# Performance work log

Measured on AMD Instinct MI355X. Metric: run time of the kernel, lower is better.

Reference implementation:

```python
import jax, jax.numpy as jnp
import numpy as np

B, L, C, OUT = 8, 256, 512, 512


def setup_inputs() -> dict:
    key = jax.random.key(0)
    ks = jax.random.split(key, 8)
    xd = jax.random.normal(ks[0], (B, L, C), jnp.float32)
    xt = jax.random.normal(ks[1], (B, L, C), jnp.float32)
    # Linear weights stored (in, out): y = x @ W + b (equiv. to torch x @ W^T)
    Wc = jax.random.normal(ks[2], (C, C), jnp.float32) * 0.02
    bc = jnp.zeros((C,), jnp.float32)
    Wp = jax.random.normal(ks[3], (C, C), jnp.float32) * 0.02
    bp = jnp.zeros((C,), jnp.float32)
    Wf = jax.random.normal(ks[4], (C, OUT), jnp.float32) * 0.02
    bf = jnp.zeros((OUT,), jnp.float32)
    return {"xd": xd, "xt": xt, "Wc": Wc, "bc": bc, "Wp": Wp, "bp": bp, "Wf": Wf, "bf": bf}


def reference(xd, xt, Wc, bc, Wp, bp, Wf, bf):
    # projected features
    pt = jax.nn.relu(xt) @ Wp + bp              # (b, Lt, C)
    pc = jax.nn.relu(xd) @ Wc + bc              # (b, Ld, C)
    # sigmoid bilinear scores: (b, Lt, Ld) == (b, Ld, Lt) since Lt == Ld structurally
    scores = jax.nn.sigmoid(jnp.einsum('bic,bkc->bik', pt, pc))
    # normalize by total per-batch sum
    w = scores / jnp.sum(scores, axis=(1, 2), keepdims=True)
    # tanh of elementwise outer product, reduced with attention weights
    # cp[b,c] = sum_{i,j} tanh(xd[b,i,c] * xt[b,j,c]) * w[b,i,j]
    cp = jnp.einsum('bijc,bij->bc', jnp.tanh(xd[:, :, None, :] * xt[:, None, :, :]), w)
    return cp @ Wf + bf
```

## Files before the change

kernel.cpp:

```cpp
#include <hip/hip_runtime.h>
#include <math.h>

#define B_   8
#define L_   256
#define C_   512
#define OUT_ 512

typedef _Float16 half8 __attribute__((ext_vector_type(8)));
typedef float    f32x4 __attribute__((ext_vector_type(4)));

__global__ __launch_bounds__(256)
void wconv_kernel(const float* __restrict__ Wp, const float* __restrict__ Wc,
                  _Float16* __restrict__ hWp, _Float16* __restrict__ hWc)
{
    const int which = blockIdx.z;
    const float* __restrict__ W = which ? Wc : Wp;
    _Float16* __restrict__ H    = which ? hWc : hWp;
    __shared__ float tl[32][33];
    const int k0 = blockIdx.y << 5, n0 = blockIdx.x << 5;
    const int tr = threadIdx.x >> 5, tc = threadIdx.x & 31;
    #pragma unroll
    for (int i = 0; i < 32; i += 8)
        tl[tr + i][tc] = W[(size_t)(k0 + tr + i) * C_ + n0 + tc];
    __syncthreads();
    #pragma unroll
    for (int i = 0; i < 32; i += 8)
        H[(size_t)(n0 + tr + i) * C_ + k0 + tc] = (_Float16)tl[tc][tr + i];
}

__global__ __launch_bounds__(256)
void proj_mfma_kernel(const float* __restrict__ xt, const _Float16* __restrict__ hWp,
                      const float* __restrict__ bp,
                      const float* __restrict__ xd, const _Float16* __restrict__ hWc,
                      const float* __restrict__ bc,
                      _Float16* __restrict__ pt, _Float16* __restrict__ pc)
{
    const int which = blockIdx.z;
    const float*    __restrict__ X    = which ? xd : xt;
    const _Float16* __restrict__ W    = which ? hWc : hWp;
    const float*    __restrict__ bias = which ? bc : bp;
    _Float16*       __restrict__ Y    = which ? pc : pt;

    __shared__ _Float16 Ah[2][64][40];
    __shared__ _Float16 Bh[2][64][40];
    __shared__ _Float16 Ot[64][72];

    const int tid = threadIdx.x;
    const int m0 = blockIdx.y << 6, n0 = blockIdx.x << 6;
    const int srow = tid >> 2, sch = (tid & 3) << 3;
    const int lane = tid & 63, wv = tid >> 6;
    const int l15 = lane & 15, quad = lane >> 4;

    const float*    Ag = X + (size_t)(m0 + srow) * C_ + sch;
    const _Float16* Bg = W + (size_t)(n0 + srow) * C_ + sch;

    float4 a0 = *(const float4*)(Ag);
    float4 a1 = *(const float4*)(Ag + 4);
    half8  bv = *(const half8*)(Bg);

    {
        half8 av;
        av[0] = (_Float16)fmaxf(a0.x, 0.f); av[1] = (_Float16)fmaxf(a0.y, 0.f);
        av[2] = (_Float16)fmaxf(a0.z, 0.f); av[3] = (_Float16)fmaxf(a0.w, 0.f);
        av[4] = (_Float16)fmaxf(a1.x, 0.f); av[5] = (_Float16)fmaxf(a1.y, 0.f);
        av[6] = (_Float16)fmaxf(a1.z, 0.f); av[7] = (_Float16)fmaxf(a1.w, 0.f);
        *(half8*)&Ah[0][srow][sch] = av;
        *(half8*)&Bh[0][srow][sch] = bv;
    }

    f32x4 acc[4] = {};
    for (int ks = 0; ks < 16; ++ks) {
        const int cur = ks & 1;
        if (ks < 15) {
            Ag += 32; Bg += 32;
            a0 = *(const float4*)(Ag);
            a1 = *(const float4*)(Ag + 4);
            bv = *(const half8*)(Bg);
        }
        __syncthreads();
        half8 af = *(const half8*)&Ah[cur][(wv << 4) + l15][quad << 3];
        #pragma unroll
        for (int nb = 0; nb < 4; ++nb) {
            half8 bf = *(const half8*)&Bh[cur][(nb << 4) + l15][quad << 3];
            acc[nb] = __builtin_amdgcn_mfma_f32_16x16x32_f16(af, bf, acc[nb], 0, 0, 0);
        }
        if (ks < 15) {
            half8 av;
            av[0] = (_Float16)fmaxf(a0.x, 0.f); av[1] = (_Float16)fmaxf(a0.y, 0.f);
            av[2] = (_Float16)fmaxf(a0.z, 0.f); av[3] = (_Float16)fmaxf(a0.w, 0.f);
            av[4] = (_Float16)fmaxf(a1.x, 0.f); av[5] = (_Float16)fmaxf(a1.y, 0.f);
            av[6] = (_Float16)fmaxf(a1.z, 0.f); av[7] = (_Float16)fmaxf(a1.w, 0.f);
            *(half8*)&Ah[cur ^ 1][srow][sch] = av;
            *(half8*)&Bh[cur ^ 1][srow][sch] = bv;
        }
    }

    __syncthreads();
    #pragma unroll
    for (int nb = 0; nb < 4; ++nb) {
        const float bz = bias[n0 + (nb << 4) + l15];
        #pragma unroll
        for (int r = 0; r < 4; ++r)
            Ot[(wv << 4) + (quad << 2) + r][(nb << 4) + l15] = (_Float16)(acc[nb][r] + bz);
    }
    __syncthreads();
    const int erow = tid >> 3, ech = (tid & 7) << 3;
    #pragma unroll
    for (int h = 0; h < 64; h += 32)
        *(half8*)&Y[(size_t)(m0 + erow + h) * C_ + n0 + ech] = *(const half8*)&Ot[erow + h][ech];
}

__global__ __launch_bounds__(256)
void sc_gemm_mfma_kernel(const _Float16* __restrict__ pt, const _Float16* __restrict__ pc,
                         float* __restrict__ dotb)
{
    const int b = blockIdx.z >> 2, ks4 = blockIdx.z & 3;
    const _Float16* __restrict__ A  = pt + (size_t)b * L_ * C_ + (ks4 << 7);
    const _Float16* __restrict__ Bm = pc + (size_t)b * L_ * C_ + (ks4 << 7);
    float* __restrict__ D = dotb + (size_t)ks4 * (B_ * L_ * L_) + (size_t)b * (L_ * L_);

    __shared__ _Float16 Ah[2][64][40];
    __shared__ _Float16 Bh[2][64][40];

    const int tid = threadIdx.x;
    const int m0 = blockIdx.y << 6, n0 = blockIdx.x << 6;
    const int srow = tid >> 2, sch = (tid & 3) << 3;
    const int lane = tid & 63, wv = tid >> 6;
    const int l15 = lane & 15, quad = lane >> 4;

    const _Float16* Ag = A  + (size_t)(m0 + srow) * C_ + sch;
    const _Float16* Bg = Bm + (size_t)(n0 + srow) * C_ + sch;

    half8 av = *(const half8*)Ag;
    half8 bv = *(const half8*)Bg;
    *(half8*)&Ah[0][srow][sch] = av;
    *(half8*)&Bh[0][srow][sch] = bv;

    f32x4 acc[4] = {};
    for (int t = 0; t < 4; ++t) {
        const int cur = t & 1;
        if (t < 3) {
            Ag += 32; Bg += 32;
            av = *(const half8*)Ag;
            bv = *(const half8*)Bg;
        }
        __syncthreads();
        half8 af = *(const half8*)&Ah[cur][(wv << 4) + l15][quad << 3];
        #pragma unroll
        for (int nb = 0; nb < 4; ++nb) {
            half8 bf = *(const half8*)&Bh[cur][(nb << 4) + l15][quad << 3];
            acc[nb] = __builtin_amdgcn_mfma_f32_16x16x32_f16(af, bf, acc[nb], 0, 0, 0);
        }
        if (t < 3) {
            *(half8*)&Ah[cur ^ 1][srow][sch] = av;
            *(half8*)&Bh[cur ^ 1][srow][sch] = bv;
        }
    }
    #pragma unroll
    for (int nb = 0; nb < 4; ++nb)
        #pragma unroll
        for (int r = 0; r < 4; ++r)
            D[(size_t)(m0 + (wv << 4) + (quad << 2) + r) * L_ + n0 + (nb << 4) + l15] = acc[nb][r];
}

__global__ __launch_bounds__(256)
void sc_finish_kernel(float* __restrict__ dotb, float* __restrict__ sums_part)
{
    __shared__ float red[256];
    const int bl = blockIdx.x;
    const int b  = bl >> 6;
    const size_t off = (size_t)b * (L_ * L_) + (size_t)((bl & 63) << 10) + ((size_t)threadIdx.x << 2);
    float4 d = *(const float4*)&dotb[off];
    #pragma unroll
    for (int k = 1; k < 4; ++k) {
        float4 e = *(const float4*)&dotb[(size_t)k * (B_ * L_ * L_) + off];
        d.x += e.x; d.y += e.y; d.z += e.z; d.w += e.w;
    }
    float4 s;
    s.x = 1.0f / (1.0f + expf(-d.x));
    s.y = 1.0f / (1.0f + expf(-d.y));
    s.z = 1.0f / (1.0f + expf(-d.z));
    s.w = 1.0f / (1.0f + expf(-d.w));
    *(float4*)&dotb[off] = s;
    red[threadIdx.x] = (s.x + s.y) + (s.z + s.w);
    __syncthreads();
    for (int st = 128; st > 0; st >>= 1) {
        if (threadIdx.x < st) red[threadIdx.x] += red[threadIdx.x + st];
        __syncthreads();
    }
    if (threadIdx.x == 0) sums_part[bl] = red[0];
}

__device__ __forceinline__ float sig2r(float a) {
    float e = __builtin_amdgcn_exp2f(a);
    return __builtin_amdgcn_rcpf(e + 1.0f);
}

__global__ __launch_bounds__(256, 4)
void cp_partial_kernel(const float* __restrict__ xd, const float* __restrict__ xt,
                       const float* __restrict__ scores, float* __restrict__ partials)
{
    const int i0  = blockIdx.x << 5;
    const int j0  = blockIdx.y << 4;
    const int b   = blockIdx.z >> 1;
    const int tid = threadIdx.x;
    const int c   = ((blockIdx.z & 1) << 8) | tid;

    __shared__ float ws_[16][36];

    const float* __restrict__ sb = scores + (size_t)b * L_ * L_;
    {
        const int jj = tid & 15;
        const int ib = (tid >> 4) << 1;
        #pragma unroll
        for (int r = 0; r < 2; ++r)
            ws_[jj][ib + r] = sb[(size_t)(i0 + ib + r) * L_ + j0 + jj];
    }

    float xds[32], xtv[16];
    const float* __restrict__ xdb = xd + ((size_t)(b * L_ + i0)) * C_ + c;
    const float* __restrict__ xtb = xt + ((size_t)(b * L_ + j0)) * C_ + c;
    #pragma unroll
    for (int i = 0; i < 32; ++i)
        xds[i] = xdb[(size_t)i * C_] * 2.8853900817779268f;
    #pragma unroll
    for (int j = 0; j < 16; ++j)
        xtv[j] = xtb[(size_t)j * C_];
    __syncthreads();

    float a0 = 0.f, a1 = 0.f, a2 = 0.f, a3 = 0.f;
    #pragma unroll 2
    for (int jj = 0; jj < 16; ++jj) {
        const float xv = xtv[jj];
        #pragma unroll
        for (int i = 0; i < 32; i += 4) {
            const float4 w4 = *(const float4*)&ws_[jj][i];
            a0 = fmaf(w4.x, sig2r(xds[i + 0] * xv), a0);
            a1 = fmaf(w4.y, sig2r(xds[i + 1] * xv), a1);
            a2 = fmaf(w4.z, sig2r(xds[i + 2] * xv), a2);
            a3 = fmaf(w4.w, sig2r(xds[i + 3] * xv), a3);
        }
    }
    const int p = ((int)blockIdx.x << 4) | (int)blockIdx.y;
    partials[(size_t)((b << 7) | p) * C_ + c] = (a0 + a1) + (a2 + a3);
}

__global__ __launch_bounds__(512)
void finalize_kernel(const float* __restrict__ partials, const float* __restrict__ sums_part,
                     const float* __restrict__ Wf, const float* __restrict__ bfv,
                     float* __restrict__ out)
{
    const int b = blockIdx.y;
    const int t = threadIdx.x;
    __shared__ float cp[C_];
    __shared__ float red[512];
    __shared__ float sumsh;

    red[t] = (t < 64) ? sums_part[(b << 6) | t] : 0.f;

    float s = 0.f;
    #pragma unroll
    for (int p = 0; p < 128; ++p)
        s += partials[(size_t)((b << 7) | p) * C_ + t];

    __syncthreads();
    for (int st = 256; st > 0; st >>= 1) {
        if (t < st) red[t] += red[t + st];
        __syncthreads();
    }
    if (t == 0) sumsh = red[0];
    __syncthreads();

    cp[t] = 1.0f - 2.0f * s / sumsh;
    __syncthreads();

    const int o  = ((int)blockIdx.x << 6) | (t & 63);
    const int c0 = (t >> 6) << 6;
    float acc = 0.f;
    #pragma unroll 8
    for (int i = 0; i < 64; ++i) {
        const int cc = c0 + i;
        acc = fmaf(cp[cc], Wf[(size_t)cc * OUT_ + o], acc);
    }
    red[t] = acc;
    __syncthreads();
    if (t < 64) {
        float a = 0.f;
        #pragma unroll
        for (int g = 0; g < 8; ++g) a += red[(g << 6) | t];
        out[(size_t)b * OUT_ + o] = a + bfv[o];
    }
}

extern "C" void kernel_launch(void* const* d_in, const int* in_sizes, int n_in,
                              void* d_out, int out_size, void* d_ws, size_t ws_size,
                              hipStream_t stream)
{
    const float* xd = (const float*)d_in[0];
    const float* xt = (const float*)d_in[1];
    const float* Wc = (const float*)d_in[2];
    const float* bc = (const float*)d_in[3];
    const float* Wp = (const float*)d_in[4];
    const float* bp = (const float*)d_in[5];
    const float* Wf = (const float*)d_in[6];
    const float* bf = (const float*)d_in[7];
    float* out = (float*)d_out;

    _Float16* hWp = (_Float16*)d_ws;
    _Float16* hWc = hWp + 262144;
    _Float16* pt  = hWc + 262144;
    _Float16* pc  = pt + 1048576;
    float* dotb      = (float*)(pc + 1048576);
    float* sums_part = dotb + 4 * (B_ * L_ * L_);
    float* partials  = (float*)pt;

    wconv_kernel<<<dim3(16, 16, 2), 256, 0, stream>>>(Wp, Wc, hWp, hWc);
    proj_mfma_kernel<<<dim3(8, 32, 2), 256, 0, stream>>>(xt, hWp, bp, xd, hWc, bc, pt, pc);
    sc_gemm_mfma_kernel<<<dim3(4, 4, 32), 256, 0, stream>>>(pt, pc, dotb);
    sc_finish_kernel<<<512, 256, 0, stream>>>(dotb, sums_part);
    cp_partial_kernel<<<dim3(8, 16, 16), 256, 0, stream>>>(xd, xt, dotb, partials);
    finalize_kernel<<<dim3(8, 8), 512, 0, stream>>>(partials, sums_part, Wf, bf, out);
}
```

Baseline: 153.9 us.

## Fuse score GEMM, sigmoid, sum and cp partial reduction into one kernel

Replaces the split-K score GEMM, the sigmoid/sum finish kernel and the cp partial kernel with a single kernel. Each block computes its 32x32 score tile with MFMA, applies the sigmoid, writes per-block sums, then runs the tanh-weighted reduction over all 512 channels. The tile becomes 32x32 in place of 32x16, which halves the number of partials. It also shares one reciprocal between two sigmoid evaluations. This removes the round trip of the 4-way split-K dot buffer through global memory and two launches, but only 4 of the 8 waves do MFMA work and the GEMM is serialized over 16 K-steps.

```diff
diff --git a/kernel.cpp b/kernel.cpp
--- a/kernel.cpp
+++ b/kernel.cpp
@@ -7,6 +7,7 @@
 #define OUT_ 512
 
 typedef _Float16 half8 __attribute__((ext_vector_type(8)));
+typedef _Float16 half4 __attribute__((ext_vector_type(4)));
 typedef float    f32x4 __attribute__((ext_vector_type(4)));
 
 __global__ __launch_bounds__(256)
@@ -110,139 +111,104 @@
         *(half8*)&Y[(size_t)(m0 + erow + h) * C_ + n0 + ech] = *(const half8*)&Ot[erow + h][ech];
 }
 
-__global__ __launch_bounds__(256)
-void sc_gemm_mfma_kernel(const _Float16* __restrict__ pt, const _Float16* __restrict__ pc,
-                         float* __restrict__ dotb)
-{
-    const int b = blockIdx.z >> 2, ks4 = blockIdx.z & 3;
-    const _Float16* __restrict__ A  = pt + (size_t)b * L_ * C_ + (ks4 << 7);
-    const _Float16* __restrict__ Bm = pc + (size_t)b * L_ * C_ + (ks4 << 7);
-    float* __restrict__ D = dotb + (size_t)ks4 * (B_ * L_ * L_) + (size_t)b * (L_ * L_);
-
-    __shared__ _Float16 Ah[2][64][40];
-    __shared__ _Float16 Bh[2][64][40];
-
+__device__ __forceinline__ float sigmoid_fast(float z) {
+    float e = __builtin_amdgcn_exp2f(-1.4426950408889634f * z);
+    return __builtin_amdgcn_rcpf(e + 1.0f);
+}
+
+__global__ __launch_bounds__(512, 4)
+void cp_scores_kernel(const _Float16* __restrict__ pt, const _Float16* __restrict__ pc,
+                      const float* __restrict__ xd, const float* __restrict__ xt,
+                      float* __restrict__ partials, float* __restrict__ sums_part)
+{
+    const int bx = blockIdx.x, by = blockIdx.y, b = blockIdx.z;
+    const int i0 = bx << 5, j0 = by << 5;
     const int tid = threadIdx.x;
-    const int m0 = blockIdx.y << 6, n0 = blockIdx.x << 6;
-    const int srow = tid >> 2, sch = (tid & 3) << 3;
     const int lane = tid & 63, wv = tid >> 6;
     const int l15 = lane & 15, quad = lane >> 4;
 
-    const _Float16* Ag = A  + (size_t)(m0 + srow) * C_ + sch;
-    const _Float16* Bg = Bm + (size_t)(n0 + srow) * C_ + sch;
-
-    half8 av = *(const half8*)Ag;
-    half8 bv = *(const half8*)Bg;
-    *(half8*)&Ah[0][srow][sch] = av;
-    *(half8*)&Bh[0][srow][sch] = bv;
-
-    f32x4 acc[4] = {};
-    for (int t = 0; t < 4; ++t) {
-        const int cur = t & 1;
-        if (t < 3) {
-            Ag += 32; Bg += 32;
-            av = *(const half8*)Ag;
-            bv = *(const half8*)Bg;
-        }
+    __shared__ _Float16 Ah[2][32][40];
+    __shared__ _Float16 Bh[2][32][40];
+    __shared__ float ws_[32][36];
+    __shared__ float wred[4];
+
+    const int sHalf = tid >> 8;
+    const int srow  = (tid & 255) >> 3;
+    const int sch   = (tid & 7) << 2;
+    const _Float16* Sg = (sHalf ? pc + (size_t)(b * L_ + j0 + srow) * C_
+                                : pt + (size_t)(b * L_ + i0 + srow) * C_) + sch;
+
+    half4 v = *(const half4*)Sg;
+    if (sHalf) *(half4*)&Bh[0][srow][sch] = v; else *(half4*)&Ah[0][srow][sch] = v;
+
+    f32x4 acc = {};
+    for (int ks = 0; ks < 16; ++ks) {
+        const int cur = ks & 1;
+        if (ks < 15) { Sg += 32; v = *(const half4*)Sg; }
         __syncthreads();
-        half8 af = *(const half8*)&Ah[cur][(wv << 4) + l15][quad << 3];
-        #pragma unroll
-        for (int nb = 0; nb < 4; ++nb) {
-            half8 bf = *(const half8*)&Bh[cur][(nb << 4) + l15][quad << 3];
-            acc[nb] = __builtin_amdgcn_mfma_f32_16x16x32_f16(af, bf, acc[nb], 0, 0, 0);
-        }
-        if (t < 3) {
-            *(half8*)&Ah[cur ^ 1][srow][sch] = av;
-            *(half8*)&Bh[cur ^ 1][srow][sch] = bv;
-        }
-    }
-    #pragma unroll
-    for (int nb = 0; nb < 4; ++nb)
-        #pragma unroll
-        for (int r = 0; r < 4; ++r)
-            D[(size_t)(m0 + (wv << 4) + (quad << 2) + r) * L_ + n0 + (nb << 4) + l15] = acc[nb][r];
-}
-
-__global__ __launch_bounds__(256)
-void sc_finish_kernel(float* __restrict__ dotb, float* __restrict__ sums_part)
-{
-    __shared__ float red[256];
-    const int bl = blockIdx.x;
-    const int b  = bl >> 6;
-    const size_t off = (size_t)b * (L_ * L_) + (size_t)((bl & 63) << 10) + ((size_t)threadIdx.x << 2);
-    float4 d = *(const float4*)&dotb[off];
-    #pragma unroll
-    for (int k = 1; k < 4; ++k) {
-        float4 e = *(const float4*)&dotb[(size_t)k * (B_ * L_ * L_) + off];
-        d.x += e.x; d.y += e.y; d.z += e.z; d.w += e.w;
-    }
-    float4 s;
-    s.x = 1.0f / (1.0f + expf(-d.x));
-    s.y = 1.0f / (1.0f + expf(-d.y));
-    s.z = 1.0f / (1.0f + expf(-d.z));
-    s.w = 1.0f / (1.0f + expf(-d.w));
-    *(float4*)&dotb[off] = s;
-    red[threadIdx.x] = (s.x + s.y) + (s.z + s.w);
-    __syncthreads();
-    for (int st = 128; st > 0; st >>= 1) {
-        if (threadIdx.x < st) red[threadIdx.x] += red[threadIdx.x + st];
-        __syncthreads();
-    }
-    if (threadIdx.x == 0) sums_part[bl] = red[0];
-}
-
-__device__ __forceinline__ float sig2r(float a) {
-    float e = __builtin_amdgcn_exp2f(a);
-    return __builtin_amdgcn_rcpf(e + 1.0f);
-}
-
-__global__ __launch_bounds__(256, 4)
-void cp_partial_kernel(const float* __restrict__ xd, const float* __restrict__ xt,
-                       const float* __restrict__ scores, float* __restrict__ partials)
-{
-    const int i0  = blockIdx.x << 5;
-    const int j0  = blockIdx.y << 4;
-    const int b   = blockIdx.z >> 1;
-    const int tid = threadIdx.x;
-    const int c   = ((blockIdx.z & 1) << 8) | tid;
-
-    __shared__ float ws_[16][36];
-
-    const float* __restrict__ sb = scores + (size_t)b * L_ * L_;
-    {
-        const int jj = tid & 15;
-        const int ib = (tid >> 4) << 1;
-        #pragma unroll
-        for (int r = 0; r < 2; ++r)
-            ws_[jj][ib + r] = sb[(size_t)(i0 + ib + r) * L_ + j0 + jj];
-    }
-
-    float xds[32], xtv[16];
-    const float* __restrict__ xdb = xd + ((size_t)(b * L_ + i0)) * C_ + c;
-    const float* __restrict__ xtb = xt + ((size_t)(b * L_ + j0)) * C_ + c;
+        if (wv < 4) {
+            half8 af = *(const half8*)&Ah[cur][((wv >> 1) << 4) + l15][quad << 3];
+            half8 bf = *(const half8*)&Bh[cur][((wv & 1) << 4) + l15][quad << 3];
+            acc = __builtin_amdgcn_mfma_f32_16x16x32_f16(af, bf, acc, 0, 0, 0);
+        }
+        if (ks < 15) {
+            if (sHalf) *(half4*)&Bh[cur ^ 1][srow][sch] = v;
+            else       *(half4*)&Ah[cur ^ 1][srow][sch] = v;
+        }
+    }
+
+    float lsum = 0.f;
+    if (wv < 4) {
+        const int n = ((wv & 1) << 4) + l15;
+        const int m = ((wv >> 1) << 4) + (quad << 2);
+        float4 sg;
+        sg.x = sigmoid_fast(acc[0]);
+        sg.y = sigmoid_fast(acc[1]);
+        sg.z = sigmoid_fast(acc[2]);
+        sg.w = sigmoid_fast(acc[3]);
+        *(float4*)&ws_[n][m] = sg;
+        lsum = (sg.x + sg.y) + (sg.z + sg.w);
+    }
+    #pragma unroll
+    for (int off = 32; off; off >>= 1) lsum += __shfl_xor(lsum, off);
+    if (wv < 4 && lane == 0) wred[wv] = lsum;
+    __syncthreads();
+    if (tid == 0)
+        sums_part[(b << 6) | (bx << 3) | by] = (wred[0] + wred[1]) + (wred[2] + wred[3]);
+
+    const int c = tid;
+    const float* __restrict__ xdb = xd + (size_t)(b * L_ + i0) * C_ + c;
+    const float* __restrict__ xtb = xt + (size_t)(b * L_ + j0) * C_ + c;
+    float xds[32], xtv[32];
     #pragma unroll
     for (int i = 0; i < 32; ++i)
         xds[i] = xdb[(size_t)i * C_] * 2.8853900817779268f;
     #pragma unroll
-    for (int j = 0; j < 16; ++j)
+    for (int j = 0; j < 32; ++j)
         xtv[j] = xtb[(size_t)j * C_];
-    __syncthreads();
 
     float a0 = 0.f, a1 = 0.f, a2 = 0.f, a3 = 0.f;
-    #pragma unroll 2
-    for (int jj = 0; jj < 16; ++jj) {
+    for (int jj = 0; jj < 32; ++jj) {
         const float xv = xtv[jj];
         #pragma unroll
         for (int i = 0; i < 32; i += 4) {
             const float4 w4 = *(const float4*)&ws_[jj][i];
-            a0 = fmaf(w4.x, sig2r(xds[i + 0] * xv), a0);
-            a1 = fmaf(w4.y, sig2r(xds[i + 1] * xv), a1);
-            a2 = fmaf(w4.z, sig2r(xds[i + 2] * xv), a2);
-            a3 = fmaf(w4.w, sig2r(xds[i + 3] * xv), a3);
-        }
-    }
-    const int p = ((int)blockIdx.x << 4) | (int)blockIdx.y;
-    partials[(size_t)((b << 7) | p) * C_ + c] = (a0 + a1) + (a2 + a3);
+            float e0 = __builtin_amdgcn_exp2f(xds[i + 0] * xv);
+            float e1 = __builtin_amdgcn_exp2f(xds[i + 1] * xv);
+            float q0 = e0 + 1.0f, q1 = e1 + 1.0f;
+            float rp01 = __builtin_amdgcn_rcpf(q0 * q1);
+            a0 = fmaf(w4.x, rp01 * q1, a0);
+            a1 = fmaf(w4.y, rp01 * q0, a1);
+            float e2 = __builtin_amdgcn_exp2f(xds[i + 2] * xv);
+            float e3 = __builtin_amdgcn_exp2f(xds[i + 3] * xv);
+            float q2 = e2 + 1.0f, q3 = e3 + 1.0f;
+            float rp23 = __builtin_amdgcn_rcpf(q2 * q3);
+            a2 = fmaf(w4.z, rp23 * q3, a2);
+            a3 = fmaf(w4.w, rp23 * q2, a3);
+        }
+    }
+    const int p = (bx << 3) | by;
+    partials[(size_t)((b << 6) | p) * C_ + c] = (a0 + a1) + (a2 + a3);
 }
 
 __global__ __launch_bounds__(512)
@@ -260,8 +226,8 @@
 
     float s = 0.f;
     #pragma unroll
-    for (int p = 0; p < 128; ++p)
-        s += partials[(size_t)((b << 7) | p) * C_ + t];
+    for (int p = 0; p < 64; ++p)
+        s += partials[(size_t)((b << 6) | p) * C_ + t];
 
     __syncthreads();
     for (int st = 256; st > 0; st >>= 1) {
@@ -310,14 +276,11 @@
     _Float16* hWc = hWp + 262144;
     _Float16* pt  = hWc + 262144;
     _Float16* pc  = pt + 1048576;
-    float* dotb      = (float*)(pc + 1048576);
-    float* sums_part = dotb + 4 * (B_ * L_ * L_);
-    float* partials  = (float*)pt;
+    float* partials  = (float*)(pc + 1048576);
+    float* sums_part = partials + B_ * 64 * C_;
 
     wconv_kernel<<<dim3(16, 16, 2), 256, 0, stream>>>(Wp, Wc, hWp, hWc);
     proj_mfma_kernel<<<dim3(8, 32, 2), 256, 0, stream>>>(xt, hWp, bp, xd, hWc, bc, pt, pc);
-    sc_gemm_mfma_kernel<<<dim3(4, 4, 32), 256, 0, stream>>>(pt, pc, dotb);
-    sc_finish_kernel<<<512, 256, 0, stream>>>(dotb, sums_part);
-    cp_partial_kernel<<<dim3(8, 16, 16), 256, 0, stream>>>(xd, xt, dotb, partials);
+    cp_scores_kernel<<<dim3(8, 8, 8), 512, 0, stream>>>(pt, pc, xd, xt, partials, sums_part);
     finalize_kernel<<<dim3(8, 8), 512, 0, stream>>>(partials, sums_part, Wf, bf, out);
 }
```

After: 147.9 us. 3.8% less time.
